# Kernel tuning notes

Hardware: AMD Instinct MI355X
Metric: run time of the kernel (lower is better)

Reference implementation:

```python
import jax, jax.numpy as jnp
import numpy as np

EPS = 1e-5  # torch BatchNorm2d default eps


def _conv(x, w, b, pad):
    y = jax.lax.conv_general_dilated(
        x, w, window_strides=(1, 1), padding=[(pad, pad), (pad, pad)],
        dimension_numbers=('NCHW', 'OIHW', 'NCHW'))
    return y + b[None, :, None, None]


def _bn_train(x, gamma, beta):
    # training-mode BatchNorm2d: biased batch statistics over (N,H,W)
    m = jnp.mean(x, axis=(0, 2, 3), keepdims=True)
    v = jnp.var(x, axis=(0, 2, 3), keepdims=True)
    xn = (x - m) * jax.lax.rsqrt(v + EPS)
    return xn * gamma[None, :, None, None] + beta[None, :, None, None]


def _ncc(s, t):
    # Vectorized equivalent of the per-pixel double loop.
    # ncc[b,0,i,j] = mean(tt * ss / (tt_std * ss_std)) over (C,th,tw)
    #             = sum(tt * s_sub) / (N * tt_std * ss_std)   (since sum(tt)=0)
    b, c, sh, sw = s.shape
    th, tw = t.shape[2], t.shape[3]
    N = c * th * tw
    tt = t - jnp.mean(t, axis=(1, 2, 3), keepdims=True)
    # torch.std is unbiased (divides by N-1)
    tt_std = jnp.sqrt(jnp.sum(tt * tt, axis=(1, 2, 3), keepdims=True) / (N - 1))

    # cross[b] = valid correlation of s[b] with its own template tt[b]
    def per_sample(si, ti):
        return jax.lax.conv_general_dilated(
            si[None], ti[None], (1, 1), 'VALID',
            dimension_numbers=('NCHW', 'OIHW', 'NCHW'))[0]  # (1,h,w)

    cross = jax.vmap(per_sample)(s, tt)  # (b,1,h,w)

    # per-window mean/std of s via box-filter conv over all C channels jointly
    box = jnp.ones((1, c, th, tw), dtype=s.dtype)
    win_sum = jax.lax.conv_general_dilated(
        s, box, (1, 1), 'VALID', dimension_numbers=('NCHW', 'OIHW', 'NCHW'))
    win_sqsum = jax.lax.conv_general_dilated(
        s * s, box, (1, 1), 'VALID', dimension_numbers=('NCHW', 'OIHW', 'NCHW'))
    win_mean = win_sum / N
    ss_var = jnp.maximum(win_sqsum - N * win_mean * win_mean, 0.0) / (N - 1)
    ss_std = jnp.sqrt(ss_var)

    return cross / (N * tt_std * ss_std)  # (b,1,h,w)


def reference(s, t, w1, b1, g1, be1, w2, b2, g2, be2,
              w3, b3, g3, be3, w4, b4):
    s = _bn_train(_conv(s, w1, b1, pad=1), g1, be1)
    t = _bn_train(_conv(t, w2, b2, pad=1), g2, be2)
    ncc = _ncc(s, t)
    x = _bn_train(_conv(ncc, w3, b3, pad=0), g3, be3)
    x = jax.nn.relu(x)
    return _conv(x, w4, b4, pad=0)  # (b,2,h,w)


def setup_inputs() -> dict:
    key = jax.random.key(0)
    ks = jax.random.split(key, 12)
    C = 256
    inp = {
        's': jax.random.normal(ks[0], (16, C, 64, 64), jnp.float32),
        't': jax.random.normal(ks[1], (16, C, 16, 16), jnp.float32),
        'w1': jax.random.normal(ks[2], (C, C, 3, 3), jnp.float32) * 0.02,
        'b1': jax.random.normal(ks[3], (C,), jnp.float32) * 0.02,
        'g1': jnp.ones((C,), jnp.float32),
        'be1': jnp.zeros((C,), jnp.float32),
        'w2': jax.random.normal(ks[4], (C, C, 3, 3), jnp.float32) * 0.02,
        'b2': jax.random.normal(ks[5], (C,), jnp.float32) * 0.02,
        'g2': jnp.ones((C,), jnp.float32),
        'be2': jnp.zeros((C,), jnp.float32),
        'w3': jax.random.normal(ks[6], (1, 1, 1, 1), jnp.float32),
        'b3': jax.random.normal(ks[7], (1,), jnp.float32) * 0.02,
        'g3': jnp.ones((1,), jnp.float32),
        'be3': jnp.zeros((1,), jnp.float32),
        'w4': jax.random.normal(ks[8], (2, 1, 1, 1), jnp.float32),
        'b4': jax.random.normal(ks[9], (2,), jnp.float32) * 0.02,
    }
    return inp
```

## Files before the change

### kernel.cpp

```cpp
#include <hip/hip_runtime.h>
#include <hip/hip_bf16.h>

#define EPSV 1e-5f

constexpr int B_ = 16, C_ = 256;
constexpr int OHW_ = 49 * 49;
constexpr int NTOT = 256 * 16 * 16;
constexpr int GROUPS = 32, CPERG = 8;

typedef short bf16x8 __attribute__((ext_vector_type(8)));
typedef float f32x4 __attribute__((ext_vector_type(4)));

constexpr size_t OFF_S1 = 0;
constexpr size_t SZ_S1  = (size_t)16 * 256 * 4096;
constexpr size_t OFF_T2 = OFF_S1 + SZ_S1;
constexpr size_t SZ_T2  = (size_t)16 * 256 * 256;
constexpr size_t OFF_ST = OFF_T2 + SZ_T2;
constexpr size_t OFF_C  = OFF_ST + 2048;
constexpr size_t SPC_BYTES = (size_t)16 * 66 * 66 * 256 * 2;
constexpr size_t TPC_BYTES = (size_t)16 * 18 * 18 * 256 * 2;
constexpr size_t WR_BYTES  = (size_t)9 * 256 * 256 * 2;
constexpr size_t ZOFF  = 0;
constexpr size_t CPOFF = 131072;
constexpr size_t NCOFF = CPOFF + (size_t)GROUPS * 16 * OHW_;
constexpr size_t SATOFF = NCOFF + (size_t)16 * OHW_;

__device__ __forceinline__ void gload_lds16(const void* g, void* l) {
    __builtin_amdgcn_global_load_lds((const __attribute__((address_space(1))) unsigned int*)g,
                                     (__attribute__((address_space(3))) unsigned int*)l,
                                     16, 0, 0);
}

template<int W>
__global__ __launch_bounds__(256)
void pad_transpose(const float* __restrict__ in, __hip_bfloat16* __restrict__ outp)
{
    constexpr int PW = W + 2;
    __shared__ float tile[64][W + 1];
    int bid = blockIdx.x;
    int icg = bid & 3; bid >>= 2;
    int yp = bid % PW; bid /= PW;
    int b = bid;
    int ic0 = icg * 64;
    int tid = threadIdx.x;
    bool interior = (yp >= 1 && yp <= W);
    if (interior) {
        int y = yp - 1;
        for (int idx = tid; idx < 64 * W; idx += 256) {
            int i = idx / W, x = idx % W;
            tile[i][x] = in[(((size_t)(b * C_ + ic0 + i)) * W + y) * W + x];
        }
    }
    __syncthreads();
    for (int idx = tid; idx < PW * 16; idx += 256) {
        int xp = idx >> 4, i4 = idx & 15;
        ushort4 v = make_ushort4(0, 0, 0, 0);
        if (interior && xp >= 1 && xp <= W) {
            #pragma unroll
            for (int k = 0; k < 4; ++k) {
                __hip_bfloat16 h = __float2bfloat16(tile[i4 * 4 + k][xp - 1]);
                reinterpret_cast<unsigned short*>(&v)[k] = *reinterpret_cast<unsigned short*>(&h);
            }
        }
        *reinterpret_cast<ushort4*>(&outp[(((size_t)(b * PW) + yp) * PW + xp) * 256 + ic0 + i4 * 4]) = v;
    }
}

__global__ __launch_bounds__(256)
void weight_reorg(const float* __restrict__ w, __hip_bfloat16* __restrict__ wr)
{
    int idx = blockIdx.x * 256 + threadIdx.x;
    const float* src = w + (size_t)idx * 9;
    #pragma unroll
    for (int t = 0; t < 9; ++t)
        wr[(size_t)t * 65536 + idx] = __float2bfloat16(src[t]);
}

template<int W>
__global__ __launch_bounds__(256)
void conv_mfma(const __hip_bfloat16* __restrict__ SPc, const __hip_bfloat16* __restrict__ Wr,
               const float* __restrict__ bias, float* __restrict__ out,
               float* __restrict__ csum, float* __restrict__ csq)
{
    constexpr int PW = W + 2;
    constexpr int NPIX = W * W;
    constexpr int NT = NPIX / 128;
    __shared__ __hip_bfloat16 A_lds[128 * 32];
    __shared__ __hip_bfloat16 B_lds[128 * 32];

    int bid = blockIdx.x;
    int nt = bid % NT; bid /= NT;
    int mt = bid & 1;  bid >>= 1;
    int b  = bid;
    int tid = threadIdx.x;
    int lane = tid & 63;
    int wv = tid >> 6, wm = wv >> 1, wn = wv & 1;
    int oc0 = mt * 128, p0 = nt * 128;

    f32x4 acc[4][4];
    #pragma unroll
    for (int i = 0; i < 4; ++i)
        #pragma unroll
        for (int j = 0; j < 4; ++j)
            #pragma unroll
            for (int r = 0; r < 4; ++r) acc[i][j][r] = 0.f;

    const bf16x8* Af = reinterpret_cast<const bf16x8*>(A_lds);
    const bf16x8* Bf = reinterpret_cast<const bf16x8*>(B_lds);
    int colb = lane >> 4;
    int rA = lane & 15;

    for (int kc = 0; kc < 72; ++kc) {
        int tap = kc >> 3, icc = kc & 7;
        int ic0 = icc * 32;
        int dy = tap / 3, dx = tap - dy * 3;
        __syncthreads();
        #pragma unroll
        for (int it = 0; it < 2; ++it) {
            int sIdx = tid + it * 256;
            int row = sIdx >> 2, seg = sIdx & 3;
            const __hip_bfloat16* srcA =
                Wr + ((size_t)(tap * 256 + oc0 + row)) * 256 + ic0 + seg * 8;
            gload_lds16(srcA, &A_lds[sIdx * 8]);
            int p = p0 + row;
            int y = p / W, x = p % W;
            const __hip_bfloat16* srcB =
                SPc + (((size_t)(b * PW + y + dy)) * PW + x + dx) * 256 + ic0 + seg * 8;
            gload_lds16(srcB, &B_lds[sIdx * 8]);
        }
        asm volatile("s_waitcnt vmcnt(0)" ::: "memory");
        __syncthreads();

        bf16x8 a[4], bb[4];
        #pragma unroll
        for (int mi = 0; mi < 4; ++mi)
            a[mi] = Af[(wm * 64 + mi * 16 + rA) * 4 + colb];
        #pragma unroll
        for (int ni = 0; ni < 4; ++ni)
            bb[ni] = Bf[(wn * 64 + ni * 16 + rA) * 4 + colb];
        #pragma unroll
        for (int mi = 0; mi < 4; ++mi)
            #pragma unroll
            for (int ni = 0; ni < 4; ++ni)
                acc[mi][ni] = __builtin_amdgcn_mfma_f32_16x16x32_bf16(
                    a[mi], bb[ni], acc[mi][ni], 0, 0, 0);
    }

    #pragma unroll
    for (int mi = 0; mi < 4; ++mi) {
        int ocb = oc0 + wm * 64 + mi * 16 + (lane >> 4) * 4;
        #pragma unroll
        for (int r = 0; r < 4; ++r) {
            int oc = ocb + r;
            float bv = bias[oc];
            float* orow = out + ((size_t)(b * C_ + oc)) * NPIX;
            float s_oc = 0.f, q_oc = 0.f;
            #pragma unroll
            for (int ni = 0; ni < 4; ++ni) {
                int px = p0 + wn * 64 + ni * 16 + (lane & 15);
                float v = acc[mi][ni][r] + bv;
                orow[px] = v;
                s_oc += v; q_oc += v * v;
            }
            #pragma unroll
            for (int m_ = 1; m_ < 16; m_ <<= 1) {
                s_oc += __shfl_xor(s_oc, m_);
                q_oc += __shfl_xor(q_oc, m_);
            }
            if ((lane & 15) == 0) {
                atomicAdd(&csum[oc], s_oc);
                atomicAdd(&csq[oc], q_oc);
            }
        }
    }
}

__device__ inline void blk_reduce2(float& a, float& q, int tid) {
    #pragma unroll
    for (int off = 32; off > 0; off >>= 1) {
        a += __shfl_down(a, off);
        q += __shfl_down(q, off);
    }
    __shared__ float ra[4], rq[4];
    if ((tid & 63) == 0) { ra[tid >> 6] = a; rq[tid >> 6] = q; }
    __syncthreads();
    if (tid == 0) { a = ra[0] + ra[1] + ra[2] + ra[3]; q = rq[0] + rq[1] + rq[2] + rq[3]; }
}

__global__ __launch_bounds__(256)
void bn_norm(float* __restrict__ x, const float* __restrict__ csum,
             const float* __restrict__ csq, const float* __restrict__ g,
             const float* __restrict__ be, int HW, int total4, float inv_cnt)
{
    int i = blockIdx.x * 256 + threadIdx.x;
    if (i >= total4) return;
    int c = ((i * 4) / HW) % C_;
    float m = csum[c] * inv_cnt;
    float v = csq[c] * inv_cnt - m * m;
    float sc = rsqrtf(v + EPSV) * g[c];
    float sh = be[c] - m * sc;
    float4 val = reinterpret_cast<float4*>(x)[i];
    val.x = val.x * sc + sh;
    val.y = val.y * sc + sh;
    val.z = val.z * sc + sh;
    val.w = val.w * sc + sh;
    reinterpret_cast<float4*>(x)[i] = val;
}

__global__ __launch_bounds__(256)
void zplane_kernel(const float* __restrict__ s1, const float* __restrict__ csum,
                   const float* __restrict__ csq, const float* __restrict__ g1,
                   const float* __restrict__ be1, float* __restrict__ z)
{
    __shared__ float SC[256], SH[256];
    int tid = threadIdx.x;
    {
        float m = csum[tid] * (1.f / 65536.f);
        float v = csq[tid] * (1.f / 65536.f) - m * m;
        float sc = rsqrtf(v + EPSV) * g1[tid];
        SC[tid] = sc; SH[tid] = be1[tid] - m * sc;
    }
    __syncthreads();
    int i = blockIdx.x * 256 + tid;
    int b = i >> 12, p = i & 4095;
    const float* base = s1 + (size_t)b * (C_ * 4096) + p;
    float s = 0.f, q = 0.f;
    for (int c = 0; c < C_; ++c) {
        float val = base[(size_t)c * 4096] * SC[c] + SH[c];
        s += val; q += val * val;
    }
    z[i] = s; z[65536 + i] = q;
}

__global__ __launch_bounds__(256)
void sat_kernel(const float* __restrict__ zin, float* __restrict__ sat)
{
    __shared__ float t[65][66];
    int pl = blockIdx.x;
    int tid = threadIdx.x;
    const float* src = zin + (size_t)pl * 4096;
    for (int idx = tid; idx < 4096; idx += 256) {
        int y = idx >> 6, x = idx & 63;
        t[y + 1][x + 1] = src[idx];
    }
    for (int idx = tid; idx < 65; idx += 256) { t[0][idx] = 0.f; t[idx][0] = 0.f; }
    __syncthreads();
    if (tid < 64) {
        float run = 0.f;
        for (int x = 1; x <= 64; ++x) { run += t[tid + 1][x]; t[tid + 1][x] = run; }
    }
    __syncthreads();
    if (tid < 64) {
        float run = 0.f;
        for (int y = 1; y <= 64; ++y) { run += t[y][tid + 1]; t[y][tid + 1] = run; }
    }
    __syncthreads();
    float* dst = sat + (size_t)pl * 4225;
    for (int idx = tid; idx < 4225; idx += 256) {
        int r = idx / 65, c = idx % 65;
        dst[idx] = t[r][c];
    }
}

__global__ __launch_bounds__(256)
void tstat_kernel(const float* __restrict__ t2, float* __restrict__ tmean, float* __restrict__ ttstd)
{
    int b = blockIdx.x, tid = threadIdx.x;
    const float* p = t2 + (size_t)b * NTOT;
    float s = 0.f, q = 0.f;
    for (int i = tid; i < NTOT; i += 256) { float v = p[i]; s += v; q += v * v; }
    blk_reduce2(s, q, tid);
    if (tid == 0) {
        float m = s / (float)NTOT;
        tmean[b] = m;
        ttstd[b] = sqrtf(fmaxf(q - (float)NTOT * m * m, 0.f) / (float)(NTOT - 1));
    }
}

__global__ __launch_bounds__(256, 2)
void cross_v3(const float* __restrict__ s1, const float* __restrict__ t2,
              const float* __restrict__ csum, const float* __restrict__ csq,
              const float* __restrict__ g1, const float* __restrict__ be1,
              float* __restrict__ cpart)
{
    __shared__ float4 spl4[1024];
    __shared__ float tpl[256];
    __shared__ float red[4][64][49];

    int g = blockIdx.x & (GROUPS - 1);
    int b = blockIdx.x / GROUPS;
    int tid = threadIdx.x;
    int phase = tid >> 6;
    int lane = tid & 63;
    int i = lane;
    int i_ld = i < 49 ? i : 48;

    float acc[49];
    #pragma unroll
    for (int j = 0; j < 49; ++j) acc[j] = 0.f;

    #pragma unroll 1
    for (int cc = 0; cc < CPERG; ++cc) {
        int c = g * CPERG + cc;
        float m = csum[c] * (1.f / 65536.f);
        float v = csq[c] * (1.f / 65536.f) - m * m;
        float sc = rsqrtf(v + EPSV) * g1[c];
        float sh = be1[c] - m * sc;
        __syncthreads();
        const float4* sp4 = reinterpret_cast<const float4*>(s1 + ((size_t)(b * C_ + c)) * 4096);
        #pragma unroll
        for (int k = 0; k < 4; ++k) {
            int gidx = tid + k * 256;
            float4 val = sp4[gidx];
            val.x = val.x * sc + sh; val.y = val.y * sc + sh;
            val.z = val.z * sc + sh; val.w = val.w * sc + sh;
            int row = gidx >> 4, jg = gidx & 15;
            spl4[row * 16 + (jg ^ (row & 7))] = val;
        }
        tpl[tid] = t2[((size_t)(b * C_ + c)) * 256 + tid];
        __syncthreads();
        #pragma unroll 1
        for (int tyl = 0; tyl < 4; ++tyl) {
            int ty = phase * 4 + tyl;
            int row = i_ld + ty;
            float r_[64];
            #pragma unroll
            for (int jg = 0; jg < 16; ++jg) {
                float4 v4 = spl4[row * 16 + (jg ^ (row & 7))];
                r_[jg * 4 + 0] = v4.x; r_[jg * 4 + 1] = v4.y;
                r_[jg * 4 + 2] = v4.z; r_[jg * 4 + 3] = v4.w;
            }
            float tt[16];
            const float4* tp4 = reinterpret_cast<const float4*>(&tpl[ty * 16]);
            #pragma unroll
            for (int k = 0; k < 4; ++k) {
                float4 tv = tp4[k];
                tt[k * 4 + 0] = tv.x; tt[k * 4 + 1] = tv.y;
                tt[k * 4 + 2] = tv.z; tt[k * 4 + 3] = tv.w;
            }
            #pragma unroll
            for (int tx = 0; tx < 16; ++tx)
                #pragma unroll
                for (int j = 0; j < 49; ++j)
                    acc[j] += tt[tx] * r_[j + tx];
        }
    }
    __syncthreads();
    if (i < 49) {
        #pragma unroll
        for (int j = 0; j < 49; ++j) red[phase][i][j] = acc[j];
    }
    __syncthreads();
    float* dst = cpart + ((size_t)(g * B_ + b)) * OHW_;
    for (int e = tid; e < OHW_; e += 256) {
        int ii = e / 49, jj = e - ii * 49;
        dst[e] = red[0][ii][jj] + red[1][ii][jj] + red[2][ii][jj] + red[3][ii][jj];
    }
}

__global__ __launch_bounds__(256)
void ncc_kernel(const float* __restrict__ cpart, const float* __restrict__ sat,
                const float* __restrict__ tmean, const float* __restrict__ ttstd,
                float* __restrict__ ncc, float* __restrict__ s3)
{
    int idx = blockIdx.x * 256 + threadIdx.x;
    float val = 0.f;
    if (idx < B_ * OHW_) {
        int b = idx / OHW_, r = idx - b * OHW_;
        int i = r / 49, j = r - i * 49;
        float cr = 0.f;
        #pragma unroll 4
        for (int g = 0; g < GROUPS; ++g) cr += cpart[((size_t)(g * B_ + b)) * OHW_ + r];
        const float* sz = sat + (size_t)b * 4225;
        const float* sq = sat + (size_t)(16 + b) * 4225;
        int a00 = i * 65 + j, a01 = i * 65 + j + 16;
        int a10 = (i + 16) * 65 + j, a11 = (i + 16) * 65 + j + 16;
        float wsum = sz[a11] - sz[a01] - sz[a10] + sz[a00];
        float wq   = sq[a11] - sq[a01] - sq[a10] + sq[a00];
        float crosst = cr - tmean[b] * wsum;
        float ssvar = fmaxf(wq - wsum * wsum * (1.f / 65536.f), 0.f) * (1.f / 65535.f);
        float ssstd = sqrtf(ssvar);
        val = crosst / (65536.f * ttstd[b] * ssstd);
        ncc[idx] = val;
    }
    float s = val, q = val * val;
    blk_reduce2(s, q, threadIdx.x);
    if (threadIdx.x == 0) { atomicAdd(&s3[0], s); atomicAdd(&s3[1], q); }
}

__global__ __launch_bounds__(256)
void final_kernel(const float* __restrict__ ncc, const float* __restrict__ s3,
                  const float* __restrict__ w3, const float* __restrict__ b3,
                  const float* __restrict__ g3, const float* __restrict__ be3,
                  const float* __restrict__ w4, const float* __restrict__ b4,
                  float* __restrict__ out)
{
    int idx = blockIdx.x * 256 + threadIdx.x;
    if (idx >= B_ * OHW_) return;
    constexpr float M = (float)(B_ * OHW_);
    float mn = s3[0] / M;
    float vn = s3[1] / M - mn * mn;
    float W3 = w3[0], B3 = b3[0];
    float my = W3 * mn + B3;
    float vy = W3 * W3 * vn;
    float sc = rsqrtf(vy + EPSV) * g3[0];
    float y = (W3 * ncc[idx] + B3 - my) * sc + be3[0];
    float h = fmaxf(y, 0.f);
    int b = idx / OHW_, r = idx - b * OHW_;
    out[((size_t)(b * 2 + 0)) * OHW_ + r] = h * w4[0] + b4[0];
    out[((size_t)(b * 2 + 1)) * OHW_ + r] = h * w4[1] + b4[1];
}

extern "C" void kernel_launch(void* const* d_in, const int* in_sizes, int n_in,
                              void* d_out, int out_size, void* d_ws, size_t ws_size,
                              hipStream_t stream)
{
    const float* s   = (const float*)d_in[0];
    const float* t   = (const float*)d_in[1];
    const float* w1  = (const float*)d_in[2];
    const float* b1  = (const float*)d_in[3];
    const float* g1  = (const float*)d_in[4];
    const float* be1 = (const float*)d_in[5];
    const float* w2  = (const float*)d_in[6];
    const float* b2  = (const float*)d_in[7];
    const float* g2  = (const float*)d_in[8];
    const float* be2 = (const float*)d_in[9];
    const float* w3  = (const float*)d_in[10];
    const float* b3  = (const float*)d_in[11];
    const float* g3  = (const float*)d_in[12];
    const float* be3 = (const float*)d_in[13];
    const float* w4  = (const float*)d_in[14];
    const float* b4  = (const float*)d_in[15];

    float* ws = (float*)d_ws;
    float* S1 = ws + OFF_S1;
    float* T2 = ws + OFF_T2;
    float* ST = ws + OFF_ST;
    float* CHS1 = ST + 0;
    float* CHQ1 = ST + 256;
    float* CHS2 = ST + 512;
    float* CHQ2 = ST + 768;
    float* S3   = ST + 1024;
    float* TM   = ST + 1040;
    float* TSD  = ST + 1056;

    char* Cb = (char*)(ws + OFF_C);
    __hip_bfloat16* SPc = (__hip_bfloat16*)Cb;
    __hip_bfloat16* TPc = (__hip_bfloat16*)(Cb + SPC_BYTES);
    __hip_bfloat16* Wr1 = (__hip_bfloat16*)(Cb + SPC_BYTES + TPC_BYTES);
    __hip_bfloat16* Wr2 = (__hip_bfloat16*)(Cb + SPC_BYTES + TPC_BYTES + WR_BYTES);
    float* Cf = (float*)Cb;
    float* Z   = Cf + ZOFF;
    float* CP  = Cf + CPOFF;
    float* NC  = Cf + NCOFF;
    float* SAT = Cf + SATOFF;

    hipMemsetAsync(ST, 0, 1026 * sizeof(float), stream);

    pad_transpose<64><<<dim3(16 * 66 * 4), dim3(256), 0, stream>>>(s, SPc);
    pad_transpose<16><<<dim3(16 * 18 * 4), dim3(256), 0, stream>>>(t, TPc);
    weight_reorg<<<dim3(256), dim3(256), 0, stream>>>(w1, Wr1);
    weight_reorg<<<dim3(256), dim3(256), 0, stream>>>(w2, Wr2);

    conv_mfma<64><<<dim3(16 * 2 * 32), dim3(256), 0, stream>>>(SPc, Wr1, b1, S1, CHS1, CHQ1);
    conv_mfma<16><<<dim3(16 * 2 * 2),  dim3(256), 0, stream>>>(TPc, Wr2, b2, T2, CHS2, CHQ2);

    bn_norm<<<dim3(1024), dim3(256), 0, stream>>>(T2, CHS2, CHQ2, g2, be2, 256, 262144, 1.f / 4096.f);
    tstat_kernel<<<dim3(16), dim3(256), 0, stream>>>(T2, TM, TSD);

    zplane_kernel<<<dim3(256), dim3(256), 0, stream>>>(S1, CHS1, CHQ1, g1, be1, Z);
    sat_kernel<<<dim3(32), dim3(256), 0, stream>>>(Z, SAT);

    cross_v3<<<dim3(16 * GROUPS), dim3(256), 0, stream>>>(S1, T2, CHS1, CHQ1, g1, be1, CP);
    ncc_kernel<<<dim3(151), dim3(256), 0, stream>>>(CP, SAT, TM, TSD, NC, S3);
    final_kernel<<<dim3(151), dim3(256), 0, stream>>>(NC, S3, w3, b3, g3, be3, w4, b4, (float*)d_out);
}
```

Measured before the change: 488.6 us.

## Double-buffer conv MFMA LDS loads, swizzle LDS, remap blocks, vectorize zplane

The MFMA convolution now double-buffers its A/B LDS tiles so the next K-chunk's global-to-LDS loads overlap the current chunk's MFMAs. It also XOR-swizzles the LDS segment layout to reduce bank conflicts, remaps block IDs across 8 chunks (likely to group work per XCD for cache locality), and sets an occupancy hint in launch bounds. Separately, zplane_kernel processes float4 per thread with a quarter of the blocks. Doubling LDS use may lower occupancy, and the smaller zplane grid may leave much of the GPU idle.

```diff
diff --git a/kernel.cpp b/kernel.cpp
--- a/kernel.cpp
+++ b/kernel.cpp
@@ -77,7 +77,7 @@
 }
 
 template<int W>
-__global__ __launch_bounds__(256)
+__global__ __launch_bounds__(256, 4)
 void conv_mfma(const __hip_bfloat16* __restrict__ SPc, const __hip_bfloat16* __restrict__ Wr,
                const float* __restrict__ bias, float* __restrict__ out,
                float* __restrict__ csum, float* __restrict__ csq)
@@ -85,13 +85,15 @@
     constexpr int PW = W + 2;
     constexpr int NPIX = W * W;
     constexpr int NT = NPIX / 128;
-    __shared__ __hip_bfloat16 A_lds[128 * 32];
-    __shared__ __hip_bfloat16 B_lds[128 * 32];
-
-    int bid = blockIdx.x;
-    int nt = bid % NT; bid /= NT;
-    int mt = bid & 1;  bid >>= 1;
-    int b  = bid;
+    constexpr int NWG = 16 * 2 * NT;
+    constexpr int CHUNK = NWG / 8;
+    __shared__ __hip_bfloat16 A_lds[2][128 * 32];
+    __shared__ __hip_bfloat16 B_lds[2][128 * 32];
+
+    int logical = (blockIdx.x & 7) * CHUNK + (blockIdx.x >> 3);
+    int nt = logical % NT; logical /= NT;
+    int mt = logical & 1;  logical >>= 1;
+    int b  = logical;
     int tid = threadIdx.x;
     int lane = tid & 63;
     int wv = tid >> 6, wm = wv >> 1, wn = wv & 1;
@@ -105,45 +107,65 @@
             #pragma unroll
             for (int r = 0; r < 4; ++r) acc[i][j][r] = 0.f;
 
-    const bf16x8* Af = reinterpret_cast<const bf16x8*>(A_lds);
-    const bf16x8* Bf = reinterpret_cast<const bf16x8*>(B_lds);
     int colb = lane >> 4;
     int rA = lane & 15;
-
-    for (int kc = 0; kc < 72; ++kc) {
+    int s_row[2], s_seg[2];
+    #pragma unroll
+    for (int it = 0; it < 2; ++it) {
+        int sIdx = tid + it * 256;
+        s_row[it] = sIdx >> 2;
+        s_seg[it] = (sIdx & 3) ^ (s_row[it] & 3);
+    }
+
+    auto STAGE = [&](int buf, int kc) {
         int tap = kc >> 3, icc = kc & 7;
         int ic0 = icc * 32;
         int dy = tap / 3, dx = tap - dy * 3;
-        __syncthreads();
         #pragma unroll
         for (int it = 0; it < 2; ++it) {
             int sIdx = tid + it * 256;
-            int row = sIdx >> 2, seg = sIdx & 3;
+            int row = s_row[it], sw = s_seg[it];
             const __hip_bfloat16* srcA =
-                Wr + ((size_t)(tap * 256 + oc0 + row)) * 256 + ic0 + seg * 8;
-            gload_lds16(srcA, &A_lds[sIdx * 8]);
+                Wr + ((size_t)(tap * 256 + oc0 + row)) * 256 + ic0 + sw * 8;
+            gload_lds16(srcA, &A_lds[buf][sIdx * 8]);
             int p = p0 + row;
             int y = p / W, x = p % W;
             const __hip_bfloat16* srcB =
-                SPc + (((size_t)(b * PW + y + dy)) * PW + x + dx) * 256 + ic0 + seg * 8;
-            gload_lds16(srcB, &B_lds[sIdx * 8]);
-        }
-        asm volatile("s_waitcnt vmcnt(0)" ::: "memory");
-        __syncthreads();
-
+                SPc + (((size_t)(b * PW + y + dy)) * PW + x + dx) * 256 + ic0 + sw * 8;
+            gload_lds16(srcB, &B_lds[buf][sIdx * 8]);
+        }
+    };
+
+    STAGE(0, 0);
+    asm volatile("s_waitcnt vmcnt(0)" ::: "memory");
+    __syncthreads();
+
+    for (int kc = 0; kc < 72; ++kc) {
+        int cur = kc & 1;
+        if (kc + 1 < 72) STAGE(cur ^ 1, kc + 1);
+
+        const bf16x8* Af = reinterpret_cast<const bf16x8*>(A_lds[cur]);
+        const bf16x8* Bf = reinterpret_cast<const bf16x8*>(B_lds[cur]);
         bf16x8 a[4], bb[4];
         #pragma unroll
-        for (int mi = 0; mi < 4; ++mi)
-            a[mi] = Af[(wm * 64 + mi * 16 + rA) * 4 + colb];
-        #pragma unroll
-        for (int ni = 0; ni < 4; ++ni)
-            bb[ni] = Bf[(wn * 64 + ni * 16 + rA) * 4 + colb];
+        for (int mi = 0; mi < 4; ++mi) {
+            int rowA = wm * 64 + mi * 16 + rA;
+            a[mi] = Af[rowA * 4 + (colb ^ (rowA & 3))];
+        }
+        #pragma unroll
+        for (int ni = 0; ni < 4; ++ni) {
+            int rowB = wn * 64 + ni * 16 + rA;
+            bb[ni] = Bf[rowB * 4 + (colb ^ (rowB & 3))];
+        }
         #pragma unroll
         for (int mi = 0; mi < 4; ++mi)
             #pragma unroll
             for (int ni = 0; ni < 4; ++ni)
                 acc[mi][ni] = __builtin_amdgcn_mfma_f32_16x16x32_bf16(
                     a[mi], bb[ni], acc[mi][ni], 0, 0, 0);
+
+        asm volatile("s_waitcnt vmcnt(0)" ::: "memory");
+        __syncthreads();
     }
 
     #pragma unroll
@@ -221,15 +243,20 @@
         SC[tid] = sc; SH[tid] = be1[tid] - m * sc;
     }
     __syncthreads();
-    int i = blockIdx.x * 256 + tid;
-    int b = i >> 12, p = i & 4095;
-    const float* base = s1 + (size_t)b * (C_ * 4096) + p;
-    float s = 0.f, q = 0.f;
+    int i4 = blockIdx.x * 256 + tid;
+    int b = i4 >> 10, p4 = i4 & 1023;
+    const float4* base = reinterpret_cast<const float4*>(s1 + (size_t)b * (C_ * 4096)) + p4;
+    float4 s = make_float4(0.f, 0.f, 0.f, 0.f);
+    float4 q = make_float4(0.f, 0.f, 0.f, 0.f);
     for (int c = 0; c < C_; ++c) {
-        float val = base[(size_t)c * 4096] * SC[c] + SH[c];
-        s += val; q += val * val;
-    }
-    z[i] = s; z[65536 + i] = q;
+        float4 v = base[(size_t)c * 1024];
+        float sc = SC[c], sh = SH[c];
+        float vx = v.x * sc + sh, vy = v.y * sc + sh, vz = v.z * sc + sh, vw = v.w * sc + sh;
+        s.x += vx; s.y += vy; s.z += vz; s.w += vw;
+        q.x += vx * vx; q.y += vy * vy; q.z += vz * vz; q.w += vw * vw;
+    }
+    reinterpret_cast<float4*>(z)[i4] = s;
+    reinterpret_cast<float4*>(z + 65536)[i4] = q;
 }
 
 __global__ __launch_bounds__(256)
@@ -468,7 +495,7 @@
     bn_norm<<<dim3(1024), dim3(256), 0, stream>>>(T2, CHS2, CHQ2, g2, be2, 256, 262144, 1.f / 4096.f);
     tstat_kernel<<<dim3(16), dim3(256), 0, stream>>>(T2, TM, TSD);
 
-    zplane_kernel<<<dim3(256), dim3(256), 0, stream>>>(S1, CHS1, CHQ1, g1, be1, Z);
+    zplane_kernel<<<dim3(64), dim3(256), 0, stream>>>(S1, CHS1, CHQ1, g1, be1, Z);
     sat_kernel<<<dim3(32), dim3(256), 0, stream>>>(Z, SAT);
 
     cross_v3<<<dim3(16 * GROUPS), dim3(256), 0, stream>>>(S1, T2, CHS1, CHQ1, g1, be1, CP);
```

Result: no change. 492.2 us (+0.7%).
